# Kernel optimization log

Hardware: AMD Instinct MI355X
Metric: run time of the kernel (lower is better)

The kernel has to match this reference:

```python
import jax, jax.numpy as jnp
import numpy as np

D_MODEL = 1024
NUM_HEADS = 16
D_K = D_MODEL // NUM_HEADS
HEADS_DIST = [4, 4, 2, 2, 4]  # [token, statement, data_flow, control_flow, standard]
HYP_DF = 5.0
HYP_CF = 5.0
NEG_INF = -1000000000.0
B, S = 4, 1024


def _head_group_weights():
    # one-hot-per-group weight vectors of length NUM_HEADS
    ws = []
    start = 0
    for n in HEADS_DIST:
        w = np.zeros(NUM_HEADS, dtype=np.float32)
        w[start:start + n] = 1.0
        ws.append(jnp.asarray(w))
        start += n
    return ws  # tok_w, stmt_w, df_w, cf_w, std_w


def setup_inputs() -> dict:
    key = jax.random.key(0)
    ks = jax.random.split(key, 12)
    f32 = jnp.float32
    inp = {
        'Q': jax.random.normal(ks[0], (B, S, D_MODEL), f32),
        'K': jax.random.normal(ks[1], (B, S, D_MODEL), f32),
        'V': jax.random.normal(ks[2], (B, S, D_MODEL), f32),
        'token': jax.random.randint(ks[3], (B, S, S), 0, 2).astype(f32),
        'statement': jax.random.randint(ks[4], (B, S, S), 0, 2).astype(f32),
        'data_flow': jax.random.randint(ks[5], (B, S, S), 0, 2).astype(f32),
        'control_flow': jax.random.randint(ks[6], (B, S, S), 0, 2).astype(f32),
        'zero_matrix': jnp.zeros((B, S, S), f32),
        'mask': jax.random.randint(ks[7], (B, 1, S, S), 0, 2).astype(jnp.int32),
        # linear layer params (torch nn.Linear: y = x @ W.T + b)
        'Wq': jax.random.normal(ks[8], (D_MODEL, D_MODEL), f32) * 0.02,
        'bq': jnp.zeros((D_MODEL,), f32),
        'Wk': jax.random.normal(ks[9], (D_MODEL, D_MODEL), f32) * 0.02,
        'bk': jnp.zeros((D_MODEL,), f32),
        'Wv': jax.random.normal(ks[10], (D_MODEL, D_MODEL), f32) * 0.02,
        'bv': jnp.zeros((D_MODEL,), f32),
        'Wo': jax.random.normal(ks[11], (D_MODEL, D_MODEL), f32) * 0.02,
        'bo': jnp.zeros((D_MODEL,), f32),
    }
    return inp


def _split_heads(x):
    b, s, _ = x.shape
    return x.reshape(b, s, NUM_HEADS, D_K).transpose(0, 2, 1, 3)  # (B,H,S,dk)


def reference(Q, K, V, token, statement, data_flow, control_flow, zero_matrix,
              mask, Wq, bq, Wk, bk, Wv, bv, Wo, bo):
    tok_w, stmt_w, df_w, cf_w, _ = _head_group_weights()

    Qh = _split_heads(Q @ Wq.T + bq)
    Kh = _split_heads(K @ Wk.T + bk)
    Vh = _split_heads(V @ Wv.T + bv)

    scores = jnp.einsum('bhqd,bhkd->bhqk', Qh, Kh) / jnp.sqrt(jnp.float32(D_K))

    # local mask: -1e9 * token for token-heads, -1e9 * statement for statement-heads,
    # zero_matrix (zeros) elsewhere — expressed via per-head group weights instead of
    # the original redundant stack.
    w = lambda v: v[None, :, None, None]  # (1,H,1,1)
    local_mask = NEG_INF * (w(tok_w) * token[:, None] + w(stmt_w) * statement[:, None])
    # global enhance: |scores * (hyp_df*data_flow | hyp_cf*control_flow)| on their heads
    enhance_adj = (HYP_DF * w(df_w) * data_flow[:, None]
                   + HYP_CF * w(cf_w) * control_flow[:, None])
    global_enhance = jnp.abs(enhance_adj * scores)

    scores = scores + local_mask + global_enhance
    scores = jnp.where(mask == 0, NEG_INF, scores)

    probs = jax.nn.softmax(scores, axis=-1)  # (B,H,S,S)
    ctx = jnp.einsum('bhqk,bhkd->bhqd', probs, Vh)
    out = ctx.transpose(0, 2, 1, 3).reshape(B, S, D_MODEL)
    return out @ Wo.T + bo
```

## Files before the change

kernel.cpp:

```cpp
#include <hip/hip_runtime.h>
#include <stdint.h>

typedef unsigned short u16;
typedef unsigned int   u32;
typedef unsigned char  u8;
typedef __attribute__((ext_vector_type(4))) float f32x4;
typedef __attribute__((ext_vector_type(8))) __bf16 bf16x8;
typedef __attribute__((ext_vector_type(2))) unsigned int u32x2;
typedef __attribute__((ext_vector_type(4))) unsigned int u32x4;

#define MFMA16(a, b, c) __builtin_amdgcn_mfma_f32_16x16x32_bf16((a), (b), (c), 0, 0, 0)

__device__ __forceinline__ u16 f2bf(float f) {
  u32 u = __float_as_uint(f);
  return (u16)((u + 0x7fffu + ((u >> 16) & 1u)) >> 16);
}

__device__ __forceinline__ void gl_lds16(const void* g, void* l) {
  __builtin_amdgcn_global_load_lds((const __attribute__((address_space(1))) u32*)g,
                                   (__attribute__((address_space(3))) u32*)l, 16, 0, 0);
}

__device__ __forceinline__ u32 cvtpk(float a, float b) {
  u32 r;
  asm("v_cvt_pk_bf16_f32 %0, %1, %2" : "=v"(r) : "v"(a), "v"(b));
  return r;
}

__device__ __forceinline__ float exp2_hw(float x) {
  float r;
  asm("v_exp_f32 %0, %1" : "=v"(r) : "v"(x));
  return r;
}

__device__ __forceinline__ void plswap32(u32& x, u32& y) {
  u32x2 r = __builtin_amdgcn_permlane32_swap(x, y, false, false);
  x = r.x; y = r.y;
}
__device__ __forceinline__ void plswap16(u32& x, u32& y) {
  u32x2 r = __builtin_amdgcn_permlane16_swap(x, y, false, false);
  x = r.x; y = r.y;
}

__device__ __forceinline__ u32 pbit(float t, float s, float d, float c, int m) {
  const u32 nm = (m == 0) ? 1u : 0u;
  u32 r = (t != 0.0f ? 1u : 0u) | (s != 0.0f ? 2u : 0u) | (d != 0.0f ? 4u : 0u) |
          (c != 0.0f ? 8u : 0u) | ((1u - nm) << 4);
  r |= (((t != 0.0f ? 1u : 0u) | nm) << 5) | (((s != 0.0f ? 1u : 0u) | nm) << 6) | (nm << 7);
  return r;
}

__global__ void __launch_bounds__(256) prep_kernel(
    const float4* __restrict__ tok, const float4* __restrict__ st, const float4* __restrict__ df,
    const float4* __restrict__ cf, const int4* __restrict__ msk, u32* __restrict__ pko,
    const float4* __restrict__ Q, const float4* __restrict__ K, const float4* __restrict__ V,
    const float4* __restrict__ Wq, const float4* __restrict__ Wk, const float4* __restrict__ Wv,
    const float4* __restrict__ Wo, ushort4* __restrict__ oQ, ushort4* __restrict__ oK,
    ushort4* __restrict__ oV, ushort4* __restrict__ oWq, ushort4* __restrict__ oWk,
    ushort4* __restrict__ oWv, ushort4* __restrict__ oWo) {
  const int bid = blockIdx.x;
  if (bid < 4096) {
    const int i = bid * 256 + threadIdx.x;
    const int b = i >> 18, rem = i & 262143, q = rem >> 8, k4 = rem & 255;
    const int t = k4 >> 4, nk = (k4 >> 2) & 3, lg = k4 & 3;
    const u32 widx = ((u32)(b * 64 + (q >> 4)) * 16 + t) * 256 + (q & 15) * 16 + lg * 4 + nk;
    float4 vt = tok[i], vs = st[i], vd = df[i], vc = cf[i];
    int4 vm = msk[i];
    u32 b0 = pbit(vt.x, vs.x, vd.x, vc.x, vm.x);
    u32 b1 = pbit(vt.y, vs.y, vd.y, vc.y, vm.y);
    u32 b2 = pbit(vt.z, vs.z, vd.z, vc.z, vm.z);
    u32 b3 = pbit(vt.w, vs.w, vd.w, vc.w, vm.w);
    pko[widx] = b0 | (b1 << 8) | (b2 << 16) | (b3 << 24);
  } else {
    const int cb = bid - 4096;
    const float4* src;
    ushort4* dst;
    int base;
    if (cb < 1024)      { src = Q;  dst = oQ;  base = cb; }
    else if (cb < 2048) { src = K;  dst = oK;  base = cb - 1024; }
    else if (cb < 3072) { src = V;  dst = oV;  base = cb - 2048; }
    else if (cb < 3328) { src = Wq; dst = oWq; base = cb - 3072; }
    else if (cb < 3584) { src = Wk; dst = oWk; base = cb - 3328; }
    else if (cb < 3840) { src = Wv; dst = oWv; base = cb - 3584; }
    else                { src = Wo; dst = oWo; base = cb - 3840; }
    const int i0 = base * 1024 + threadIdx.x;
#pragma unroll
    for (int u = 0; u < 4; u++) {
      const int i = i0 + u * 256;
      float4 v = src[i];
      dst[i] = make_ushort4(f2bf(v.x), f2bf(v.y), f2bf(v.z), f2bf(v.w));
    }
  }
}

__global__ void __launch_bounds__(256) gemm_qkv(const u16* __restrict__ Abase, const u16* __restrict__ Wbase,
                                                const float* __restrict__ bq, const float* __restrict__ bk,
                                                const float* __restrict__ bv, u16* __restrict__ Obase) {
  __shared__ u16 smA[2][4096];
  __shared__ u16 smB[2][4096];
  const int fb = blockIdx.x;
  const int lid = (fb & 7) * 96 + (fb >> 3);
  const int z = lid >> 8;
  const int m0 = ((lid & 255) >> 3) * 128;
  const int n0 = (lid & 7) * 128;
  const u16* A = Abase + (size_t)z * 4194304;
  const u16* W = Wbase + (size_t)z * 1048576;
  const float* bias = (z == 0) ? bq : (z == 1) ? bk : bv;
  u16* Out = Obase + (size_t)z * 4194304;
  const int t = threadIdx.x;
  const int w = t >> 6, l = t & 63;
  const int l15 = l & 15, lg = l >> 4;
  const int wr = w >> 1, wc = w & 1;
  f32x4 acc[4][4] = {};
  const int srow = w * 16 + (l >> 2);
  const int scol_src = (((l & 3) ^ ((l >> 2) & 3))) * 8;
  const int scol_dst = (l & 3) * 8;
  const u16* Ab = A + (size_t)(m0 + srow) * 1024 + scol_src;
  const u16* Wb = W + (size_t)(n0 + srow) * 1024 + scol_src;
  const int soff = srow * 32 + scol_dst;
  const int c0g = (lg ^ (l15 & 3)) * 8;

  gl_lds16(Ab, &smA[0][soff]);
  gl_lds16(Ab + (size_t)64 * 1024, &smA[0][soff + 64 * 32]);
  gl_lds16(Wb, &smB[0][soff]);
  gl_lds16(Wb + (size_t)64 * 1024, &smB[0][soff + 64 * 32]);

  for (int it = 0; it < 32; it++) {
    __syncthreads();
    if (it < 31) {
      const int kk = (it + 1) * 32;
      const int nb = (it + 1) & 1;
      gl_lds16(Ab + kk, &smA[nb][soff]);
      gl_lds16(Ab + kk + (size_t)64 * 1024, &smA[nb][soff + 64 * 32]);
      gl_lds16(Wb + kk, &smB[nb][soff]);
      gl_lds16(Wb + kk + (size_t)64 * 1024, &smB[nb][soff + 64 * 32]);
    }
    const u16* bA = smA[it & 1];
    const u16* bB = smB[it & 1];
    bf16x8 af[4], bv_[4];
#pragma unroll
    for (int i = 0; i < 4; i++) af[i] = *(const bf16x8*)(bA + (wr * 64 + i * 16 + l15) * 32 + c0g);
#pragma unroll
    for (int i = 0; i < 4; i++) bv_[i] = *(const bf16x8*)(bB + (wc * 64 + i * 16 + l15) * 32 + c0g);
#pragma unroll
    for (int i = 0; i < 4; i++)
#pragma unroll
      for (int j = 0; j < 4; j++) acc[i][j] = MFMA16(af[i], bv_[j], acc[i][j]);
  }
#pragma unroll
  for (int j = 0; j < 4; j++) {
    const int n = n0 + wc * 64 + j * 16 + l15;
    const float bvj = bias[n];
#pragma unroll
    for (int i = 0; i < 4; i++) {
      const int mbase = m0 + wr * 64 + i * 16 + lg * 4;
      if (z < 2) {
#pragma unroll
        for (int r = 0; r < 4; r++) {
          const int m = mbase + r;
          Out[((size_t)((m >> 10) * 16 + (n >> 6)) << 16) + (size_t)(m & 1023) * 64 + (n & 63)] =
              f2bf(acc[i][j][r] + bvj);
        }
      } else {
        size_t off = ((size_t)((mbase >> 10) * 16 + (n >> 6)) << 16) + (size_t)(n & 63) * 1024 + (mbase & 1023);
        *(ushort4*)(Out + off) = make_ushort4(f2bf(acc[i][j][0] + bvj), f2bf(acc[i][j][1] + bvj),
                                              f2bf(acc[i][j][2] + bvj), f2bf(acc[i][j][3] + bvj));
      }
    }
  }
}

__global__ void __launch_bounds__(256) gemm_out(const u16* __restrict__ A, const u16* __restrict__ W,
                                                const float* __restrict__ bias, float* __restrict__ Out) {
  __shared__ u16 smA[2][4096];
  __shared__ u16 smB[2][4096];
  const int fb = blockIdx.x;
  const int lid = (fb & 7) * 32 + (fb >> 3);
  const int m0 = (lid >> 3) * 128;
  const int n0 = (lid & 7) * 128;
  const int t = threadIdx.x;
  const int w = t >> 6, l = t & 63;
  const int l15 = l & 15, lg = l >> 4;
  const int wr = w >> 1, wc = w & 1;
  f32x4 acc[4][4] = {};
  const int srow = w * 16 + (l >> 2);
  const int scol_src = (((l & 3) ^ ((l >> 2) & 3))) * 8;
  const int scol_dst = (l & 3) * 8;
  const u16* Ab = A + (size_t)(m0 + srow) * 1024 + scol_src;
  const u16* Wb = W + (size_t)(n0 + srow) * 1024 + scol_src;
  const int soff = srow * 32 + scol_dst;
  const int c0g = (lg ^ (l15 & 3)) * 8;

  gl_lds16(Ab, &smA[0][soff]);
  gl_lds16(Ab + (size_t)64 * 1024, &smA[0][soff + 64 * 32]);
  gl_lds16(Wb, &smB[0][soff]);
  gl_lds16(Wb + (size_t)64 * 1024, &smB[0][soff + 64 * 32]);

  for (int it = 0; it < 32; it++) {
    __syncthreads();
    if (it < 31) {
      const int kk = (it + 1) * 32;
      const int nb = (it + 1) & 1;
      gl_lds16(Ab + kk, &smA[nb][soff]);
      gl_lds16(Ab + kk + (size_t)64 * 1024, &smA[nb][soff + 64 * 32]);
      gl_lds16(Wb + kk, &smB[nb][soff]);
      gl_lds16(Wb + kk + (size_t)64 * 1024, &smB[nb][soff + 64 * 32]);
    }
    const u16* bA = smA[it & 1];
    const u16* bB = smB[it & 1];
    bf16x8 af[4], bv_[4];
#pragma unroll
    for (int i = 0; i < 4; i++) af[i] = *(const bf16x8*)(bA + (wr * 64 + i * 16 + l15) * 32 + c0g);
#pragma unroll
    for (int i = 0; i < 4; i++) bv_[i] = *(const bf16x8*)(bB + (wc * 64 + i * 16 + l15) * 32 + c0g);
#pragma unroll
    for (int i = 0; i < 4; i++)
#pragma unroll
      for (int j = 0; j < 4; j++) acc[i][j] = MFMA16(af[i], bv_[j], acc[i][j]);
  }
#pragma unroll
  for (int j = 0; j < 4; j++) {
    const int n = n0 + wc * 64 + j * 16 + l15;
    const float bvj = bias[n];
#pragma unroll
    for (int i = 0; i < 4; i++) {
      const int mbase = m0 + wr * 64 + i * 16 + lg * 4;
#pragma unroll
      for (int r = 0; r < 4; r++) Out[(size_t)(mbase + r) * 1024 + n] = acc[i][j][r] + bvj;
    }
  }
}

__global__ void __launch_bounds__(512) attn_kernel(const u16* __restrict__ Qp, const u16* __restrict__ Kp,
                                                   const u16* __restrict__ Vt, const u8* __restrict__ pack,
                                                   u16* __restrict__ ctx) {
  __shared__ u16 smK[2][4096];
  __shared__ u16 smV[2][4096];
  const float SCL  = 0.18033688011112042f;
  const float FMX  = 32.0f;
  const int tid = threadIdx.x;
  const int w = tid >> 6, l = tid & 63;
  const int l15 = l & 15, lg = l >> 4;
  const int f = blockIdx.x;
  const int swz = (f & 7) * 64 + (f >> 3);
  const int bh = swz >> 3, bx = swz & 7;
  const int b = bh >> 4, h = bh & 15;
  const int q0 = bx * 128 + w * 16;
  const bool enh = (h >= 8 && h < 12);
  const u32 kbit = (h < 4) ? 0x20u : (h < 8) ? 0x40u : 0x80u;
  const u32 ebit = (h < 10) ? 0x04u : 0x08u;
  const u32 kb_[4] = {kbit, kbit << 8, kbit << 16, kbit << 24};
  const u32 eb_[4] = {ebit, ebit << 8, ebit << 16, ebit << 24};
  const size_t hb = (size_t)bh << 16;
  const u32x4 onesw = {0x3F803F80u, 0x3F803F80u, 0x3F803F80u, 0x3F803F80u};
  const bf16x8 ones_frag = __builtin_bit_cast(bf16x8, onesw);

  bf16x8 qf[2];
#pragma unroll
  for (int ks = 0; ks < 2; ks++)
    qf[ks] = *(const bf16x8*)(Qp + hb + (size_t)(q0 + l15) * 64 + ks * 32 + lg * 8);

  const int srow = w * 8 + (l >> 3);
  const int schunk = (l & 7) ^ (l >> 3);
  const u16* Ksrc = Kp + hb + (size_t)srow * 64 + schunk * 8;
  const u16* Vsrc = Vt + hb + (size_t)srow * 1024 + schunk * 8;
  const int c0 = (lg ^ (l15 & 7)) * 8;
  const u8* pkq = pack + ((size_t)((b * 64 + bx * 8 + w) * 16)) * 1024 + (l15 * 4 + lg) * 16;

  gl_lds16(Ksrc, &smK[0][w * 512]);
  gl_lds16(Vsrc, &smV[0][w * 512]);
  uint4 pk_next = *(const uint4*)(pkq);

  f32x4 octx[4] = {};
  f32x4 osum = {};

  for (int t = 0; t < 16; t++) {
    __syncthreads();
    const uint4 pkc = pk_next;
    if (t < 15) {
      const int kb = (t + 1) * 64;
      const int nb = (t + 1) & 1;
      gl_lds16(Ksrc + (size_t)kb * 64, &smK[nb][w * 512]);
      gl_lds16(Vsrc + kb, &smV[nb][w * 512]);
      pk_next = *(const uint4*)(pkq + (t + 1) * 1024);
    }
    const u16* bK = smK[t & 1];
    const u16* bV = smV[t & 1];
    f32x4 sc[4];
    __builtin_amdgcn_s_setprio(1);
#pragma unroll
    for (int nk = 0; nk < 4; nk++) {
      const u16* kr = bK + (nk * 16 + l15) * 64;
      bf16x8 kf0 = *(const bf16x8*)(kr + c0);
      bf16x8 kf1 = *(const bf16x8*)(kr + (c0 ^ 32));
      f32x4 z = {0.0f, 0.0f, 0.0f, 0.0f};
      z = MFMA16(kf0, qf[0], z);
      z = MFMA16(kf1, qf[1], z);
      sc[nk] = z;
    }
    __builtin_amdgcn_s_setprio(0);
    const u32 pkw[4] = {pkc.x, pkc.y, pkc.z, pkc.w};
#pragma unroll
    for (int nk = 0; nk < 4; nk++)
#pragma unroll
      for (int r = 0; r < 4; r++) {
        float s;
        if (enh) {
          float tt = sc[nk][r] * SCL;
          tt = (pkw[nk] & eb_[r]) ? __builtin_fmaf(fabsf(tt), 5.0f, tt) : tt;
          s = tt - FMX;
        } else {
          s = __builtin_fmaf(sc[nk][r], SCL, -FMX);
        }
        float p = exp2_hw(s);
        p = (pkw[nk] & kb_[r]) ? 0.0f : p;
        sc[nk][r] = p;
      }
    __builtin_amdgcn_s_setprio(1);
#pragma unroll
    for (int kk = 0; kk < 2; kk++) {
      u32 a0 = cvtpk(sc[2 * kk][0], sc[2 * kk][1]);
      u32 a1 = cvtpk(sc[2 * kk][2], sc[2 * kk][3]);
      u32 b0 = cvtpk(sc[2 * kk + 1][0], sc[2 * kk + 1][1]);
      u32 b1 = cvtpk(sc[2 * kk + 1][2], sc[2 * kk + 1][3]);
      plswap32(a0, b0);
      plswap32(a1, b1);
      plswap16(a0, b0);
      plswap16(a1, b1);
      u32x4 wv = {a0, a1, b0, b1};
      bf16x8 pfrag = __builtin_bit_cast(bf16x8, wv);
      osum = MFMA16(ones_frag, pfrag, osum);
#pragma unroll
      for (int nd = 0; nd < 4; nd++) {
        bf16x8 vf = *(const bf16x8*)(bV + (nd * 16 + l15) * 64 + (c0 ^ (kk * 32)));
        octx[nd] = MFMA16(vf, pfrag, octx[nd]);
      }
    }
    __builtin_amdgcn_s_setprio(0);
  }
  const float inv = 1.0f / fmaxf(osum[0], 1e-35f);
  u16* cb = ctx + (size_t)b * 1048576 + (size_t)(q0 + l15) * 1024 + h * 64 + lg * 4;
#pragma unroll
  for (int nd = 0; nd < 4; nd++) {
    *(ushort4*)(cb + nd * 16) = make_ushort4(f2bf(octx[nd][0] * inv), f2bf(octx[nd][1] * inv),
                                             f2bf(octx[nd][2] * inv), f2bf(octx[nd][3] * inv));
  }
}

extern "C" void kernel_launch(void* const* d_in, const int* in_sizes, int n_in,
                              void* d_out, int out_size, void* d_ws, size_t ws_size,
                              hipStream_t stream) {
  (void)in_sizes; (void)n_in; (void)out_size; (void)ws_size;
  const float* Q  = (const float*)d_in[0];
  const float* K  = (const float*)d_in[1];
  const float* V  = (const float*)d_in[2];
  const float* tok = (const float*)d_in[3];
  const float* st  = (const float*)d_in[4];
  const float* df  = (const float*)d_in[5];
  const float* cf  = (const float*)d_in[6];
  const int*   msk = (const int*)d_in[8];
  const float* Wq = (const float*)d_in[9];
  const float* bq = (const float*)d_in[10];
  const float* Wk = (const float*)d_in[11];
  const float* bk = (const float*)d_in[12];
  const float* Wv = (const float*)d_in[13];
  const float* bv = (const float*)d_in[14];
  const float* Wo = (const float*)d_in[15];
  const float* bo = (const float*)d_in[16];

  char* ws = (char*)d_ws;
  const size_t MB = 1ull << 20;
  u16* Qbf = (u16*)(ws);
  u16* Wqb = (u16*)(ws + 24 * MB);
  u8*  pkQ = (u8*)(ws + 32 * MB);
  u16* Qh  = (u16*)(ws + 36 * MB);
  u16* ctx = (u16*)(ws + 60 * MB);
  u16* Kbf = Qbf + 4194304;
  u16* Vbf = Qbf + 8388608;
  u16* Wkb = Wqb + 1048576;
  u16* Wvb = Wqb + 2097152;
  u16* Wob = Wqb + 3145728;

  prep_kernel<<<8192, 256, 0, stream>>>(
      (const float4*)tok, (const float4*)st, (const float4*)df, (const float4*)cf, (const int4*)msk, (u32*)pkQ,
      (const float4*)Q, (const float4*)K, (const float4*)V, (const float4*)Wq, (const float4*)Wk,
      (const float4*)Wv, (const float4*)Wo, (ushort4*)Qbf, (ushort4*)Kbf, (ushort4*)Vbf,
      (ushort4*)Wqb, (ushort4*)Wkb, (ushort4*)Wvb, (ushort4*)Wob);
  gemm_qkv<<<768, 256, 0, stream>>>(Qbf, Wqb, bq, bk, bv, Qh);
  attn_kernel<<<512, 512, 0, stream>>>(Qh, Qh + 4194304, Qh + 8388608, pkQ, ctx);
  gemm_out<<<256, 256, 0, stream>>>(ctx, Wob, bo, (float*)d_out);
}
```

Baseline: 127.0 us.

## Move mask bit-packing into QKV GEMM launch to overlap with matmul

Splits the prep kernel: the fp32-to-bf16 conversion becomes its own kernel, and the mask/adjacency bit-packing blocks are appended as extra blocks of the QKV projection GEMM launch. The memory-bound packing work (about 80 MB of reads) can then run alongside the compute-bound GEMM tiles instead of serially before them. In exchange, the packing blocks carry the GEMM's shared memory footprint, which can limit occupancy, and the block scheduling order decides how much overlap actually happens.

```diff
diff --git a/kernel.cpp b/kernel.cpp
--- a/kernel.cpp
+++ b/kernel.cpp
@@ -42,6 +42,33 @@
   x = r.x; y = r.y;
 }
 
+__global__ void __launch_bounds__(256) cvt_kernel(const float4* __restrict__ Q, const float4* __restrict__ K,
+                                                  const float4* __restrict__ V, const float4* __restrict__ Wq,
+                                                  const float4* __restrict__ Wk, const float4* __restrict__ Wv,
+                                                  const float4* __restrict__ Wo, ushort4* __restrict__ oQ,
+                                                  ushort4* __restrict__ oK, ushort4* __restrict__ oV,
+                                                  ushort4* __restrict__ oWq, ushort4* __restrict__ oWk,
+                                                  ushort4* __restrict__ oWv, ushort4* __restrict__ oWo) {
+  const int cb = blockIdx.x;
+  const float4* src;
+  ushort4* dst;
+  int base;
+  if (cb < 1024)      { src = Q;  dst = oQ;  base = cb; }
+  else if (cb < 2048) { src = K;  dst = oK;  base = cb - 1024; }
+  else if (cb < 3072) { src = V;  dst = oV;  base = cb - 2048; }
+  else if (cb < 3328) { src = Wq; dst = oWq; base = cb - 3072; }
+  else if (cb < 3584) { src = Wk; dst = oWk; base = cb - 3328; }
+  else if (cb < 3840) { src = Wv; dst = oWv; base = cb - 3584; }
+  else                { src = Wo; dst = oWo; base = cb - 3840; }
+  const int i0 = base * 1024 + threadIdx.x;
+#pragma unroll
+  for (int u = 0; u < 4; u++) {
+    const int i = i0 + u * 256;
+    float4 v = src[i];
+    dst[i] = make_ushort4(f2bf(v.x), f2bf(v.y), f2bf(v.z), f2bf(v.w));
+  }
+}
+
 __device__ __forceinline__ u32 pbit(float t, float s, float d, float c, int m) {
   const u32 nm = (m == 0) ? 1u : 0u;
   u32 r = (t != 0.0f ? 1u : 0u) | (s != 0.0f ? 2u : 0u) | (d != 0.0f ? 4u : 0u) |
@@ -50,17 +77,16 @@
   return r;
 }
 
-__global__ void __launch_bounds__(256) prep_kernel(
+__global__ void __launch_bounds__(256) gemm_qkv_pack(
+    const u16* __restrict__ Abase, const u16* __restrict__ Wbase, const float* __restrict__ bq,
+    const float* __restrict__ bk, const float* __restrict__ bv, u16* __restrict__ Obase,
     const float4* __restrict__ tok, const float4* __restrict__ st, const float4* __restrict__ df,
-    const float4* __restrict__ cf, const int4* __restrict__ msk, u32* __restrict__ pko,
-    const float4* __restrict__ Q, const float4* __restrict__ K, const float4* __restrict__ V,
-    const float4* __restrict__ Wq, const float4* __restrict__ Wk, const float4* __restrict__ Wv,
-    const float4* __restrict__ Wo, ushort4* __restrict__ oQ, ushort4* __restrict__ oK,
-    ushort4* __restrict__ oV, ushort4* __restrict__ oWq, ushort4* __restrict__ oWk,
-    ushort4* __restrict__ oWv, ushort4* __restrict__ oWo) {
-  const int bid = blockIdx.x;
-  if (bid < 4096) {
-    const int i = bid * 256 + threadIdx.x;
+    const float4* __restrict__ cf, const int4* __restrict__ msk, u32* __restrict__ pko) {
+  __shared__ u16 smA[2][4096];
+  __shared__ u16 smB[2][4096];
+  const int fb = blockIdx.x;
+  if (fb >= 768) {
+    const int i = (fb - 768) * 256 + threadIdx.x;
     const int b = i >> 18, rem = i & 262143, q = rem >> 8, k4 = rem & 255;
     const int t = k4 >> 4, nk = (k4 >> 2) & 3, lg = k4 & 3;
     const u32 widx = ((u32)(b * 64 + (q >> 4)) * 16 + t) * 256 + (q & 15) * 16 + lg * 4 + nk;
@@ -71,34 +97,8 @@
     u32 b2 = pbit(vt.z, vs.z, vd.z, vc.z, vm.z);
     u32 b3 = pbit(vt.w, vs.w, vd.w, vc.w, vm.w);
     pko[widx] = b0 | (b1 << 8) | (b2 << 16) | (b3 << 24);
-  } else {
-    const int cb = bid - 4096;
-    const float4* src;
-    ushort4* dst;
-    int base;
-    if (cb < 1024)      { src = Q;  dst = oQ;  base = cb; }
-    else if (cb < 2048) { src = K;  dst = oK;  base = cb - 1024; }
-    else if (cb < 3072) { src = V;  dst = oV;  base = cb - 2048; }
-    else if (cb < 3328) { src = Wq; dst = oWq; base = cb - 3072; }
-    else if (cb < 3584) { src = Wk; dst = oWk; base = cb - 3328; }
-    else if (cb < 3840) { src = Wv; dst = oWv; base = cb - 3584; }
-    else                { src = Wo; dst = oWo; base = cb - 3840; }
-    const int i0 = base * 1024 + threadIdx.x;
-#pragma unroll
-    for (int u = 0; u < 4; u++) {
-      const int i = i0 + u * 256;
-      float4 v = src[i];
-      dst[i] = make_ushort4(f2bf(v.x), f2bf(v.y), f2bf(v.z), f2bf(v.w));
-    }
-  }
-}
-
-__global__ void __launch_bounds__(256) gemm_qkv(const u16* __restrict__ Abase, const u16* __restrict__ Wbase,
-                                                const float* __restrict__ bq, const float* __restrict__ bk,
-                                                const float* __restrict__ bv, u16* __restrict__ Obase) {
-  __shared__ u16 smA[2][4096];
-  __shared__ u16 smB[2][4096];
-  const int fb = blockIdx.x;
+    return;
+  }
   const int lid = (fb & 7) * 96 + (fb >> 3);
   const int z = lid >> 8;
   const int m0 = ((lid & 255) >> 3) * 128;
@@ -381,12 +381,13 @@
   u16* Wvb = Wqb + 2097152;
   u16* Wob = Wqb + 3145728;
 
-  prep_kernel<<<8192, 256, 0, stream>>>(
-      (const float4*)tok, (const float4*)st, (const float4*)df, (const float4*)cf, (const int4*)msk, (u32*)pkQ,
-      (const float4*)Q, (const float4*)K, (const float4*)V, (const float4*)Wq, (const float4*)Wk,
-      (const float4*)Wv, (const float4*)Wo, (ushort4*)Qbf, (ushort4*)Kbf, (ushort4*)Vbf,
-      (ushort4*)Wqb, (ushort4*)Wkb, (ushort4*)Wvb, (ushort4*)Wob);
-  gemm_qkv<<<768, 256, 0, stream>>>(Qbf, Wqb, bq, bk, bv, Qh);
+  cvt_kernel<<<4096, 256, 0, stream>>>((const float4*)Q, (const float4*)K, (const float4*)V,
+                                       (const float4*)Wq, (const float4*)Wk, (const float4*)Wv, (const float4*)Wo,
+                                       (ushort4*)Qbf, (ushort4*)Kbf, (ushort4*)Vbf,
+                                       (ushort4*)Wqb, (ushort4*)Wkb, (ushort4*)Wvb, (ushort4*)Wob);
+  gemm_qkv_pack<<<4864, 256, 0, stream>>>(Qbf, Wqb, bq, bk, bv, Qh,
+                                          (const float4*)tok, (const float4*)st, (const float4*)df,
+                                          (const float4*)cf, (const int4*)msk, (u32*)pkQ);
   attn_kernel<<<512, 512, 0, stream>>>(Qh, Qh + 4194304, Qh + 8388608, pkQ, ctx);
   gemm_out<<<256, 256, 0, stream>>>(ctx, Wob, bo, (float*)d_out);
 }
```

After: 119.0 us, median of 2. -6.3%, faster.
